# Kernel optimization log

Measured on AMD Instinct MI355X. Metric: run time of the kernel, lower is better.

Reference implementation:

```python
import jax, jax.numpy as jnp
import numpy as np

H = 1024
N_HEAD = 16
HEAD = H // N_HEAD
EPS = 1e-12


def setup_inputs() -> dict:
    key = jax.random.key(0)
    ks = jax.random.split(key, 12)
    B, S = 2, 2048
    scale = 1.0 / np.sqrt(H)
    inp = {
        "pre_out": jax.random.normal(ks[0], (B, S, H), dtype=jnp.float32),
        "att_mask": jnp.ones((B, 1, 1, S), dtype=jnp.float32),
        "Wq": jax.random.normal(ks[1], (H, H), dtype=jnp.float32) * scale,
        "bq": jnp.zeros((H,), dtype=jnp.float32),
        "Wk": jax.random.normal(ks[2], (H, H), dtype=jnp.float32) * scale,
        "bk": jnp.zeros((H,), dtype=jnp.float32),
        "Wv": jax.random.normal(ks[3], (H, H), dtype=jnp.float32) * scale,
        "bv": jnp.zeros((H,), dtype=jnp.float32),
        "Wo": jax.random.normal(ks[4], (H, H), dtype=jnp.float32) * scale,
        "bo": jnp.zeros((H,), dtype=jnp.float32),
        "ln_w": jnp.ones((H,), dtype=jnp.float32),
        "ln_b": jnp.zeros((H,), dtype=jnp.float32),
    }
    return inp


def _heads(x):
    # [B,S,H] -> [B,n_head,S,head]
    B, S, _ = x.shape
    return x.reshape(B, S, N_HEAD, HEAD).transpose(0, 2, 1, 3)


def _layernorm(x, w, b):
    u = jnp.mean(x, axis=-1, keepdims=True)
    s = jnp.mean((x - u) ** 2, axis=-1, keepdims=True)
    return w * ((x - u) / jnp.sqrt(s + EPS)) + b


def reference(pre_out, att_mask, Wq, bq, Wk, bk, Wv, bv, Wo, bo, ln_w, ln_b):
    B, S, _ = pre_out.shape
    # torch Linear: y = x @ W.T + b
    Q = _heads(pre_out @ Wq.T + bq)
    K = _heads(pre_out @ Wk.T + bk)
    V = _heads(pre_out @ Wv.T + bv)
    scores = jnp.einsum('bhqd,bhkd->bhqk', Q, K) / np.sqrt(HEAD)
    scores = scores + (1.0 - att_mask) * -10000.0
    prob = jax.nn.softmax(scores, axis=-1)  # eval mode: no dropout
    att = jnp.einsum('bhqk,bhkd->bhqd', prob, V)
    att = att.transpose(0, 2, 1, 3).reshape(B, S, H)
    out = att @ Wo.T + bo
    return _layernorm(pre_out + out, ln_w, ln_b)
```

## Files before the change

kernel.cpp:

```cpp
#include <hip/hip_runtime.h>
#include <math.h>

typedef unsigned short u16;
typedef float floatx4 __attribute__((ext_vector_type(4)));
typedef __bf16 bf16x8 __attribute__((ext_vector_type(8)));
typedef u16 u16x4 __attribute__((ext_vector_type(4)));

#define BB 2
#define SS 2048
#define HH 1024
#define NHEAD 16

__device__ __forceinline__ u16 f2bf(float f) {
  union { float f; unsigned u; } a; a.f = f;
  unsigned r = a.u + 0x7fffu + ((a.u >> 16) & 1u);
  return (u16)(r >> 16);
}

__device__ __forceinline__ u16 bfbits(float f) {
  union { __bf16 h; u16 u; } c; c.h = (__bf16)f; return c.u;
}

__device__ __forceinline__ float bf2f(u16 u) {
  union { unsigned u; float f; } a; a.u = ((unsigned)u) << 16; return a.f;
}

__device__ __forceinline__ void gload16(const u16* g, u16* l) {
  __builtin_amdgcn_global_load_lds((const __attribute__((address_space(1))) void*)g,
                                   (__attribute__((address_space(3))) void*)l, 16, 0, 0);
}

__global__ __launch_bounds__(256) void cvt_all(
    const float* __restrict__ X, const float* __restrict__ Wq, const float* __restrict__ Wk,
    const float* __restrict__ Wv, const float* __restrict__ Wo, const float* __restrict__ mask,
    u16* __restrict__ Xb, u16* __restrict__ Wqb, u16* __restrict__ Wkb,
    u16* __restrict__ Wvb, u16* __restrict__ Wob, float* __restrict__ B2) {
  int i = blockIdx.x * 256 + threadIdx.x;
  if (i >= (2 << 20)) {
    int off = i - (2 << 20);
    float4 m = ((const float4*)mask)[off];
    float4 o;
    o.x = (1.0f - m.x) * (-10000.0f * 1.44269504f);
    o.y = (1.0f - m.y) * (-10000.0f * 1.44269504f);
    o.z = (1.0f - m.z) * (-10000.0f * 1.44269504f);
    o.w = (1.0f - m.w) * (-10000.0f * 1.44269504f);
    ((float4*)B2)[off] = o;
    return;
  }
  const float* src; u16* dst; int off;
  if (i < (1 << 20)) { src = X; dst = Xb; off = i; }
  else {
    int j = i - (1 << 20);
    int m = j >> 18; off = j & ((1 << 18) - 1);
    src = (m == 0) ? Wq : (m == 1) ? Wk : (m == 2) ? Wv : Wo;
    dst = (m == 0) ? Wqb : (m == 1) ? Wkb : (m == 2) ? Wvb : Wob;
  }
  float4 v = ((const float4*)src)[off];
  u16x4 p; p.x = f2bf(v.x); p.y = f2bf(v.y); p.z = f2bf(v.z); p.w = f2bf(v.w);
  ((u16x4*)dst)[off] = p;
}

__global__ __launch_bounds__(256) void qkv_gemm(
    const u16* __restrict__ X,
    const u16* __restrict__ Wq, const u16* __restrict__ Wk, const u16* __restrict__ Wv,
    const float* __restrict__ bq, const float* __restrict__ bk, const float* __restrict__ bv,
    u16* __restrict__ Qo, u16* __restrict__ Ko, u16* __restrict__ Vt) {
  __shared__ u16 As[128 * 32];
  __shared__ u16 Ws[128 * 32];

  const int tid = threadIdx.x;
  const int w = tid >> 6, lane = tid & 63, quad = lane >> 4, l15 = lane & 15;
  const int mat = blockIdx.x >> 3;
  const int col0 = (blockIdx.x & 7) * 128;
  const int row0 = blockIdx.y * 128;
  const u16* W = (mat == 0) ? Wq : (mat == 1) ? Wk : Wv;
  const float* bias = (mat == 0) ? bq : (mat == 1) ? bk : bv;

  const int c0 = tid, c1 = tid + 256;
  const int ar0 = c0 >> 2, al0 = ((c0 & 3) ^ (ar0 & 3)) * 8;
  const int ar1 = c1 >> 2, al1 = ((c1 & 3) ^ (ar1 & 3)) * 8;
  const u16* gA0 = X + (row0 + ar0) * HH + al0;
  const u16* gA1 = X + (row0 + ar1) * HH + al1;
  const u16* gW0 = W + (col0 + ar0) * HH + al0;
  const u16* gW1 = W + (col0 + ar1) * HH + al1;
  u16* lA0 = As + c0 * 8; u16* lA1 = As + c1 * 8;
  u16* lW0 = Ws + c0 * 8; u16* lW1 = Ws + c1 * 8;

  const int wm = (w >> 1) * 64, wn = (w & 1) * 64;
  const int sw = quad ^ (l15 & 3);
  const int aoff = (wm + l15) * 32 + sw * 8;
  const int boff = (wn + l15) * 32 + sw * 8;

  floatx4 acc[4][4];
#pragma unroll
  for (int i = 0; i < 4; i++)
#pragma unroll
    for (int j = 0; j < 4; j++) acc[i][j] = {0.f, 0.f, 0.f, 0.f};

  for (int k0 = 0; k0 < HH; k0 += 32) {
    __syncthreads();
    gload16(gA0 + k0, lA0);
    gload16(gA1 + k0, lA1);
    gload16(gW0 + k0, lW0);
    gload16(gW1 + k0, lW1);
    __syncthreads();
    bf16x8 af[4], bfr[4];
#pragma unroll
    for (int i = 0; i < 4; i++) af[i] = *(const bf16x8*)(As + aoff + i * 512);
#pragma unroll
    for (int j = 0; j < 4; j++) bfr[j] = *(const bf16x8*)(Ws + boff + j * 512);
#pragma unroll
    for (int i = 0; i < 4; i++)
#pragma unroll
      for (int j = 0; j < 4; j++)
        acc[i][j] = __builtin_amdgcn_mfma_f32_16x16x32_bf16(af[i], bfr[j], acc[i][j], 0, 0, 0);
  }

  const int rb = row0 + wm + quad * 4;
  if (mat < 2) {
    u16* O = (mat == 0) ? Qo : Ko;
#pragma unroll
    for (int j = 0; j < 4; j++) {
      const int col = col0 + wn + j * 16 + l15;
      const float bj = bias[col];
#pragma unroll
      for (int i = 0; i < 4; i++) {
        const int r0 = rb + i * 16;
#pragma unroll
        for (int r = 0; r < 4; r++)
          O[(r0 + r) * HH + col] = bfbits(acc[i][j][r] + bj);
      }
    }
  } else {
#pragma unroll
    for (int j = 0; j < 4; j++) {
      const int col = col0 + wn + j * 16 + l15;
      const float bj = bias[col];
      const int h = col >> 6, d = col & 63;
#pragma unroll
      for (int i = 0; i < 4; i++) {
        const int m0 = rb + i * 16;
        const int b = m0 >> 11, s = m0 & 2047;
        u16x4 pk;
#pragma unroll
        for (int r = 0; r < 4; r++) pk[r] = bfbits(acc[i][j][r] + bj);
        *(u16x4*)(Vt + (((b * NHEAD + h) * 64 + d) * SS + s)) = pk;
      }
    }
  }
}

__global__ __launch_bounds__(256) void oproj_gemm(
    const u16* __restrict__ A, const u16* __restrict__ W,
    const float* __restrict__ bias, float* __restrict__ Y) {
  __shared__ u16 As[128 * 32];
  __shared__ u16 Ws[128 * 32];

  const int tid = threadIdx.x;
  const int w = tid >> 6, lane = tid & 63, quad = lane >> 4, l15 = lane & 15;
  const int col0 = blockIdx.x * 128;
  const int row0 = blockIdx.y * 128;

  const int c0 = tid, c1 = tid + 256;
  const int ar0 = c0 >> 2, al0 = ((c0 & 3) ^ (ar0 & 3)) * 8;
  const int ar1 = c1 >> 2, al1 = ((c1 & 3) ^ (ar1 & 3)) * 8;
  const u16* gA0 = A + (row0 + ar0) * HH + al0;
  const u16* gA1 = A + (row0 + ar1) * HH + al1;
  const u16* gW0 = W + (col0 + ar0) * HH + al0;
  const u16* gW1 = W + (col0 + ar1) * HH + al1;
  u16* lA0 = As + c0 * 8; u16* lA1 = As + c1 * 8;
  u16* lW0 = Ws + c0 * 8; u16* lW1 = Ws + c1 * 8;

  const int wm = (w >> 1) * 64, wn = (w & 1) * 64;
  const int sw = quad ^ (l15 & 3);
  const int aoff = (wm + l15) * 32 + sw * 8;
  const int boff = (wn + l15) * 32 + sw * 8;

  floatx4 acc[4][4];
#pragma unroll
  for (int i = 0; i < 4; i++)
#pragma unroll
    for (int j = 0; j < 4; j++) acc[i][j] = {0.f, 0.f, 0.f, 0.f};

  for (int k0 = 0; k0 < HH; k0 += 32) {
    __syncthreads();
    gload16(gA0 + k0, lA0);
    gload16(gA1 + k0, lA1);
    gload16(gW0 + k0, lW0);
    gload16(gW1 + k0, lW1);
    __syncthreads();
    bf16x8 af[4], bfr[4];
#pragma unroll
    for (int i = 0; i < 4; i++) af[i] = *(const bf16x8*)(As + aoff + i * 512);
#pragma unroll
    for (int j = 0; j < 4; j++) bfr[j] = *(const bf16x8*)(Ws + boff + j * 512);
#pragma unroll
    for (int i = 0; i < 4; i++)
#pragma unroll
      for (int j = 0; j < 4; j++)
        acc[i][j] = __builtin_amdgcn_mfma_f32_16x16x32_bf16(af[i], bfr[j], acc[i][j], 0, 0, 0);
  }

  const int rb = row0 + wm + quad * 4;
#pragma unroll
  for (int j = 0; j < 4; j++) {
    const int col = col0 + wn + j * 16 + l15;
    const float bj = bias[col];
#pragma unroll
    for (int i = 0; i < 4; i++) {
      const int r0 = rb + i * 16;
#pragma unroll
      for (int r = 0; r < 4; r++)
        Y[(r0 + r) * HH + col] = acc[i][j][r] + bj;
    }
  }
}

#define QT 128

__global__ __launch_bounds__(256) void attn_mfma(
    const u16* __restrict__ Q, const u16* __restrict__ K, const u16* __restrict__ Vt,
    const float* __restrict__ B2,
    u16* __restrict__ Po0, u16* __restrict__ Po1,
    float* __restrict__ L0, float* __restrict__ L1) {
  __shared__ u16 UQ[9216];
  __shared__ u16 Ks[64 * 64];
  __shared__ u16 Vs[64 * 64];

  const int qt = blockIdx.x, bh = blockIdx.y, split = blockIdx.z;
  const int b = bh >> 4, h = bh & 15;
  const int tid = threadIdx.x;
  const int w = tid >> 6, lane = tid & 63, quad = lane >> 4, l15 = lane & 15;
  const int sw = l15 & 7;

  u16* Po = split ? Po1 : Po0;
  float* Lp = split ? L1 : L0;

  const int qbase  = (b * SS + qt * QT) * HH + h * 64;
  const int kvbase = (b * SS) * HH + h * 64;
  const int vtbase = (b * NHEAD + h) * 64 * SS;

#pragma unroll
  for (int i = 0; i < 4; i++) {
    const int c = tid + i * 256;
    const int r = c >> 3, lc = (c & 7) ^ (r & 7);
    gload16(Q + qbase + r * HH + lc * 8, UQ + c * 8);
  }
  __syncthreads();

  bf16x8 aQ[2][2];
#pragma unroll
  for (int mt = 0; mt < 2; mt++) {
    const u16* qr = UQ + (w * 32 + mt * 16 + l15) * 64;
    aQ[mt][0] = *(const bf16x8*)(qr + ((quad ^ sw) * 8));
    aQ[mt][1] = *(const bf16x8*)(qr + (((4 + quad) ^ sw) * 8));
  }

  floatx4 o[2][4];
  float lp[2][4];
#pragma unroll
  for (int mt = 0; mt < 2; mt++)
#pragma unroll
    for (int j = 0; j < 4; j++) o[mt][j] = {0.f, 0.f, 0.f, 0.f};
#pragma unroll
  for (int mt = 0; mt < 2; mt++)
#pragma unroll
    for (int r = 0; r < 4; r++) lp[mt][r] = 0.f;

  u16* Pw = UQ + w * 2304;
  const float* B2row = B2 + b * SS;

  const int kt0 = split * 16;
  for (int kt = kt0; kt < kt0 + 16; kt++) {
    __syncthreads();
#pragma unroll
    for (int i = 0; i < 2; i++) {
      const int c = tid + i * 256;
      const int r = c >> 3, lc = (c & 7) ^ (r & 7);
      gload16(K + kvbase + (kt * 64 + r) * HH + lc * 8, Ks + c * 8);
      gload16(Vt + vtbase + r * SS + kt * 64 + lc * 8, Vs + c * 8);
    }
    __syncthreads();

    floatx4 s[2][4];
#pragma unroll
    for (int j = 0; j < 4; j++) {
      const u16* kr = Ks + (j * 16 + l15) * 64;
      bf16x8 b0 = *(const bf16x8*)(kr + ((quad ^ sw) * 8));
      bf16x8 b1 = *(const bf16x8*)(kr + (((4 + quad) ^ sw) * 8));
#pragma unroll
      for (int mt = 0; mt < 2; mt++) {
        floatx4 z = {0.f, 0.f, 0.f, 0.f};
        z = __builtin_amdgcn_mfma_f32_16x16x32_bf16(aQ[mt][0], b0, z, 0, 0, 0);
        s[mt][j] = __builtin_amdgcn_mfma_f32_16x16x32_bf16(aQ[mt][1], b1, z, 0, 0, 0);
      }
    }

#pragma unroll
    for (int j = 0; j < 4; j++) {
      const float bb = B2row[kt * 64 + j * 16 + l15];
#pragma unroll
      for (int mt = 0; mt < 2; mt++)
#pragma unroll
        for (int r = 0; r < 4; r++) {
          const float p = __builtin_amdgcn_exp2f(s[mt][j][r] * 0.180336880f + bb);
          s[mt][j][r] = p;
          lp[mt][r] += p;
        }
    }

#pragma unroll
    for (int mt = 0; mt < 2; mt++)
#pragma unroll
      for (int j = 0; j < 4; j++)
#pragma unroll
        for (int r = 0; r < 4; r++)
          Pw[(mt * 16 + quad * 4 + r) * 72 + j * 16 + l15] = bfbits(s[mt][j][r]);

    bf16x8 pa[2][2];
#pragma unroll
    for (int mt = 0; mt < 2; mt++) {
      const u16* pr = Pw + (mt * 16 + l15) * 72;
      pa[mt][0] = *(const bf16x8*)(pr + quad * 8);
      pa[mt][1] = *(const bf16x8*)(pr + 32 + quad * 8);
    }
#pragma unroll
    for (int j = 0; j < 4; j++) {
      const u16* vr = Vs + (j * 16 + l15) * 64;
      bf16x8 v0 = *(const bf16x8*)(vr + ((quad ^ sw) * 8));
      bf16x8 v1 = *(const bf16x8*)(vr + (((4 + quad) ^ sw) * 8));
#pragma unroll
      for (int mt = 0; mt < 2; mt++) {
        o[mt][j] = __builtin_amdgcn_mfma_f32_16x16x32_bf16(pa[mt][0], v0, o[mt][j], 0, 0, 0);
        o[mt][j] = __builtin_amdgcn_mfma_f32_16x16x32_bf16(pa[mt][1], v1, o[mt][j], 0, 0, 0);
      }
    }
  }

#pragma unroll
  for (int mt = 0; mt < 2; mt++)
#pragma unroll
    for (int r = 0; r < 4; r++) {
      float v = lp[mt][r];
      v += __shfl_xor(v, 1); v += __shfl_xor(v, 2);
      v += __shfl_xor(v, 4); v += __shfl_xor(v, 8);
      lp[mt][r] = v;
    }

#pragma unroll
  for (int mt = 0; mt < 2; mt++) {
    const int orow0 = b * SS + qt * QT + w * 32 + mt * 16 + quad * 4;
#pragma unroll
    for (int r = 0; r < 4; r++)
#pragma unroll
      for (int j = 0; j < 4; j++)
        Po[(orow0 + r) * HH + h * 64 + j * 16 + l15] = bfbits(o[mt][j][r]);
  }
  if (l15 == 0) {
#pragma unroll
    for (int mt = 0; mt < 2; mt++) {
      const int orow0 = b * SS + qt * QT + w * 32 + mt * 16 + quad * 4;
#pragma unroll
      for (int r = 0; r < 4; r++)
        Lp[(orow0 + r) * NHEAD + h] = lp[mt][r];
    }
  }
}

__global__ __launch_bounds__(256) void attn_combine(
    const u16* __restrict__ Po1, const float* __restrict__ L0,
    const float* __restrict__ L1, u16* __restrict__ Ab ) {
  const int idx = blockIdx.x * 256 + threadIdx.x;
  const int i = idx * 4;
  const int row = i >> 10;
  const int h = (i & 1023) >> 6;
  const float inv = 1.0f / (L0[row * NHEAD + h] + L1[row * NHEAD + h]);
  u16x4 a = ((const u16x4*)Ab)[idx];
  u16x4 c = ((const u16x4*)Po1)[idx];
  u16x4 o;
#pragma unroll
  for (int k = 0; k < 4; k++) o[k] = bfbits((bf2f(a[k]) + bf2f(c[k])) * inv);
  ((u16x4*)Ab)[idx] = o;
}

__device__ __forceinline__ float block_sum256(float v) {
  __shared__ float sb[4];
#pragma unroll
  for (int o = 1; o < 64; o <<= 1) v += __shfl_xor(v, o);
  if ((threadIdx.x & 63) == 0) sb[threadIdx.x >> 6] = v;
  __syncthreads();
  float r = sb[0] + sb[1] + sb[2] + sb[3];
  __syncthreads();
  return r;
}

__global__ __launch_bounds__(256) void add_layernorm(
    const float* __restrict__ x0, const float* __restrict__ y,
    const float* __restrict__ w, const float* __restrict__ b,
    float* __restrict__ out) {
  const int row = blockIdx.x;
  const int t = threadIdx.x;
  const float* xr = x0 + (size_t)row * HH;
  const float* yr = y + (size_t)row * HH;

  float v[4];
  float sum = 0.f;
#pragma unroll
  for (int i = 0; i < 4; i++) {
    int idx = t + i * 256;
    v[i] = xr[idx] + yr[idx];
    sum += v[i];
  }
  float mean = block_sum256(sum) * (1.0f / HH);

  float sq = 0.f;
#pragma unroll
  for (int i = 0; i < 4; i++) {
    float d = v[i] - mean;
    sq += d * d;
  }
  float var = block_sum256(sq) * (1.0f / HH);
  float inv = rsqrtf(var + 1e-12f);

#pragma unroll
  for (int i = 0; i < 4; i++) {
    int idx = t + i * 256;
    out[(size_t)row * HH + idx] = w[idx] * ((v[i] - mean) * inv) + b[idx];
  }
}

extern "C" void kernel_launch(void* const* d_in, const int* in_sizes, int n_in,
                              void* d_out, int out_size, void* d_ws, size_t ws_size,
                              hipStream_t stream) {
  const float* pre_out = (const float*)d_in[0];
  const float* mask    = (const float*)d_in[1];
  const float* Wq = (const float*)d_in[2];
  const float* bq = (const float*)d_in[3];
  const float* Wk = (const float*)d_in[4];
  const float* bk = (const float*)d_in[5];
  const float* Wv = (const float*)d_in[6];
  const float* bv = (const float*)d_in[7];
  const float* Wo = (const float*)d_in[8];
  const float* bo = (const float*)d_in[9];
  const float* ln_w = (const float*)d_in[10];
  const float* ln_b = (const float*)d_in[11];
  float* out = (float*)d_out;

  u16* Xb  = (u16*)d_ws;
  u16* Wqb = Xb + (4 << 20);
  u16* Wkb = Wqb + (1 << 20);
  u16* Wvb = Wkb + (1 << 20);
  u16* Wob = Wvb + (1 << 20);
  u16* Qb  = Wob + (1 << 20);
  u16* Kb  = Qb + (4 << 20);
  u16* Vtb = Kb + (4 << 20);
  u16* Ab  = Vtb + (4 << 20);
  float* Yb = (float*)(Ab + (4 << 20));
  float* B2 = Yb + (4 << 20);

  u16* Po1  = (u16*)Yb;
  float* L0 = (float*)(Po1 + (4 << 20));
  float* L1 = L0 + (BB * SS * NHEAD);

  cvt_all<<<8196, 256, 0, stream>>>(pre_out, Wq, Wk, Wv, Wo, mask,
                                    Xb, Wqb, Wkb, Wvb, Wob, B2);

  qkv_gemm<<<dim3(24, 32), 256, 0, stream>>>(Xb, Wqb, Wkb, Wvb, bq, bk, bv, Qb, Kb, Vtb);

  attn_mfma<<<dim3(SS / QT, BB * NHEAD, 2), 256, 0, stream>>>(Qb, Kb, Vtb, B2,
                                                              Ab, Po1, L0, L1);

  attn_combine<<<4096, 256, 0, stream>>>(Po1, L0, L1, Ab);

  oproj_gemm<<<dim3(8, 32), 256, 0, stream>>>(Ab, Wob, bo, Yb);

  add_layernorm<<<BB * SS, 256, 0, stream>>>(pre_out, Yb, ln_w, ln_b, out);
}
```

Measured before the change: 239.4 us.

## Double-buffer K/V tiles and keep P in registers via transposed score MFMA

The attention kernel now double-buffers K and V tiles in shared memory, prefetching the next tile while computing the current one, which removes one barrier per iteration. It also computes S^T (K as the A operand) so each lane holds probabilities in a layout that feeds 16x16x16 bf16 MFMAs directly, dropping the LDS round trip for P. Output stores become packed 4-wide writes and the row-sum reduction shrinks to two shuffles. The costs are twice the K/V LDS footprint and twice as many smaller MFMAs for the PV product.

Result: slower. 251.0 us (+4.8%).

```diff
diff --git a/kernel.cpp b/kernel.cpp
--- a/kernel.cpp
+++ b/kernel.cpp
@@ -4,6 +4,8 @@
 typedef unsigned short u16;
 typedef float floatx4 __attribute__((ext_vector_type(4)));
 typedef __bf16 bf16x8 __attribute__((ext_vector_type(8)));
+typedef __bf16 bf16x4 __attribute__((ext_vector_type(4)));
+typedef short s16x4 __attribute__((ext_vector_type(4)));
 typedef u16 u16x4 __attribute__((ext_vector_type(4)));
 
 #define BB 2
@@ -23,6 +25,15 @@
 
 __device__ __forceinline__ float bf2f(u16 u) {
   union { unsigned u; float f; } a; a.u = ((unsigned)u) << 16; return a.f;
+}
+
+__device__ __forceinline__ floatx4 mfma16(s16x4 a, s16x4 b, floatx4 c) {
+#if __has_builtin(__builtin_amdgcn_mfma_f32_16x16x16_bf16)
+  return __builtin_amdgcn_mfma_f32_16x16x16_bf16(
+      __builtin_bit_cast(bf16x4, a), __builtin_bit_cast(bf16x4, b), c, 0, 0, 0);
+#else
+  return __builtin_amdgcn_mfma_f32_16x16x16bf16_1k(a, b, c, 0, 0, 0);
+#endif
 }
 
 __device__ __forceinline__ void gload16(const u16* g, u16* l) {
@@ -223,9 +234,9 @@
     const float* __restrict__ B2,
     u16* __restrict__ Po0, u16* __restrict__ Po1,
     float* __restrict__ L0, float* __restrict__ L1) {
-  __shared__ u16 UQ[9216];
-  __shared__ u16 Ks[64 * 64];
-  __shared__ u16 Vs[64 * 64];
+  __shared__ u16 UQ[QT * 64];
+  __shared__ u16 Ks[2][64 * 64];
+  __shared__ u16 Vs[2][64 * 64];
 
   const int qt = blockIdx.x, bh = blockIdx.y, split = blockIdx.z;
   const int b = bh >> 4, h = bh & 15;
@@ -239,6 +250,7 @@
   const int qbase  = (b * SS + qt * QT) * HH + h * 64;
   const int kvbase = (b * SS) * HH + h * 64;
   const int vtbase = (b * NHEAD + h) * 64 * SS;
+  const int kt0 = split * 16;
 
 #pragma unroll
   for (int i = 0; i < 4; i++) {
@@ -246,6 +258,13 @@
     const int r = c >> 3, lc = (c & 7) ^ (r & 7);
     gload16(Q + qbase + r * HH + lc * 8, UQ + c * 8);
   }
+#pragma unroll
+  for (int i = 0; i < 2; i++) {
+    const int c = tid + i * 256;
+    const int r = c >> 3, lc = (c & 7) ^ (r & 7);
+    gload16(K + kvbase + (kt0 * 64 + r) * HH + lc * 8, Ks[0] + c * 8);
+    gload16(Vt + vtbase + r * SS + kt0 * 64 + lc * 8, Vs[0] + c * 8);
+  }
   __syncthreads();
 
   bf16x8 aQ[2][2];
@@ -257,113 +276,90 @@
   }
 
   floatx4 o[2][4];
-  float lp[2][4];
 #pragma unroll
   for (int mt = 0; mt < 2; mt++)
 #pragma unroll
-    for (int j = 0; j < 4; j++) o[mt][j] = {0.f, 0.f, 0.f, 0.f};
-#pragma unroll
-  for (int mt = 0; mt < 2; mt++)
-#pragma unroll
-    for (int r = 0; r < 4; r++) lp[mt][r] = 0.f;
-
-  u16* Pw = UQ + w * 2304;
+    for (int dt = 0; dt < 4; dt++) o[mt][dt] = {0.f, 0.f, 0.f, 0.f};
+  float lp[2] = {0.f, 0.f};
   const float* B2row = B2 + b * SS;
 
-  const int kt0 = split * 16;
-  for (int kt = kt0; kt < kt0 + 16; kt++) {
+  for (int it = 0; it < 16; it++) {
+    const int cur = it & 1;
     __syncthreads();
-#pragma unroll
-    for (int i = 0; i < 2; i++) {
-      const int c = tid + i * 256;
-      const int r = c >> 3, lc = (c & 7) ^ (r & 7);
-      gload16(K + kvbase + (kt * 64 + r) * HH + lc * 8, Ks + c * 8);
-      gload16(Vt + vtbase + r * SS + kt * 64 + lc * 8, Vs + c * 8);
-    }
-    __syncthreads();
-
-    floatx4 s[2][4];
-#pragma unroll
-    for (int j = 0; j < 4; j++) {
-      const u16* kr = Ks + (j * 16 + l15) * 64;
-      bf16x8 b0 = *(const bf16x8*)(kr + ((quad ^ sw) * 8));
-      bf16x8 b1 = *(const bf16x8*)(kr + (((4 + quad) ^ sw) * 8));
+    if (it < 15) {
+      const int kt = kt0 + it + 1;
+#pragma unroll
+      for (int i = 0; i < 2; i++) {
+        const int c = tid + i * 256;
+        const int r = c >> 3, lc = (c & 7) ^ (r & 7);
+        gload16(K + kvbase + (kt * 64 + r) * HH + lc * 8, Ks[cur ^ 1] + c * 8);
+        gload16(Vt + vtbase + r * SS + kt * 64 + lc * 8, Vs[cur ^ 1] + c * 8);
+      }
+    }
+    const int kt = kt0 + it;
+
+    floatx4 st[2][4];
+#pragma unroll
+    for (int kb = 0; kb < 4; kb++) {
+      const u16* kr = Ks[cur] + (kb * 16 + l15) * 64;
+      bf16x8 kf0 = *(const bf16x8*)(kr + ((quad ^ sw) * 8));
+      bf16x8 kf1 = *(const bf16x8*)(kr + (((4 + quad) ^ sw) * 8));
 #pragma unroll
       for (int mt = 0; mt < 2; mt++) {
         floatx4 z = {0.f, 0.f, 0.f, 0.f};
-        z = __builtin_amdgcn_mfma_f32_16x16x32_bf16(aQ[mt][0], b0, z, 0, 0, 0);
-        s[mt][j] = __builtin_amdgcn_mfma_f32_16x16x32_bf16(aQ[mt][1], b1, z, 0, 0, 0);
+        z = __builtin_amdgcn_mfma_f32_16x16x32_bf16(kf0, aQ[mt][0], z, 0, 0, 0);
+        st[mt][kb] = __builtin_amdgcn_mfma_f32_16x16x32_bf16(kf1, aQ[mt][1], z, 0, 0, 0);
       }
     }
 
-#pragma unroll
-    for (int j = 0; j < 4; j++) {
-      const float bb = B2row[kt * 64 + j * 16 + l15];
+    s16x4 pb[2][4];
+#pragma unroll
+    for (int kb = 0; kb < 4; kb++) {
+      const floatx4 bb = *(const floatx4*)(B2row + kt * 64 + kb * 16 + quad * 4);
 #pragma unroll
       for (int mt = 0; mt < 2; mt++)
 #pragma unroll
         for (int r = 0; r < 4; r++) {
-          const float p = __builtin_amdgcn_exp2f(s[mt][j][r] * 0.180336880f + bb);
-          s[mt][j][r] = p;
-          lp[mt][r] += p;
+          const float p = __builtin_amdgcn_exp2f(st[mt][kb][r] * 0.180336880f + bb[r]);
+          lp[mt] += p;
+          pb[mt][kb][r] = (short)bfbits(p);
         }
     }
 
 #pragma unroll
-    for (int mt = 0; mt < 2; mt++)
-#pragma unroll
-      for (int j = 0; j < 4; j++)
-#pragma unroll
-        for (int r = 0; r < 4; r++)
-          Pw[(mt * 16 + quad * 4 + r) * 72 + j * 16 + l15] = bfbits(s[mt][j][r]);
-
-    bf16x8 pa[2][2];
-#pragma unroll
-    for (int mt = 0; mt < 2; mt++) {
-      const u16* pr = Pw + (mt * 16 + l15) * 72;
-      pa[mt][0] = *(const bf16x8*)(pr + quad * 8);
-      pa[mt][1] = *(const bf16x8*)(pr + 32 + quad * 8);
-    }
-#pragma unroll
-    for (int j = 0; j < 4; j++) {
-      const u16* vr = Vs + (j * 16 + l15) * 64;
-      bf16x8 v0 = *(const bf16x8*)(vr + ((quad ^ sw) * 8));
-      bf16x8 v1 = *(const bf16x8*)(vr + (((4 + quad) ^ sw) * 8));
-#pragma unroll
-      for (int mt = 0; mt < 2; mt++) {
-        o[mt][j] = __builtin_amdgcn_mfma_f32_16x16x32_bf16(pa[mt][0], v0, o[mt][j], 0, 0, 0);
-        o[mt][j] = __builtin_amdgcn_mfma_f32_16x16x32_bf16(pa[mt][1], v1, o[mt][j], 0, 0, 0);
+    for (int dt = 0; dt < 4; dt++) {
+      const u16* vr = Vs[cur] + (dt * 16 + l15) * 64;
+#pragma unroll
+      for (int kb = 0; kb < 4; kb++) {
+        const int pc = (2 * kb + (quad >> 1)) ^ sw;
+        s16x4 va = *(const s16x4*)(vr + pc * 8 + (quad & 1) * 4);
+#pragma unroll
+        for (int mt = 0; mt < 2; mt++)
+          o[mt][dt] = mfma16(va, pb[mt][kb], o[mt][dt]);
       }
     }
   }
 
 #pragma unroll
-  for (int mt = 0; mt < 2; mt++)
-#pragma unroll
-    for (int r = 0; r < 4; r++) {
-      float v = lp[mt][r];
-      v += __shfl_xor(v, 1); v += __shfl_xor(v, 2);
-      v += __shfl_xor(v, 4); v += __shfl_xor(v, 8);
-      lp[mt][r] = v;
-    }
-
-#pragma unroll
   for (int mt = 0; mt < 2; mt++) {
-    const int orow0 = b * SS + qt * QT + w * 32 + mt * 16 + quad * 4;
-#pragma unroll
-    for (int r = 0; r < 4; r++)
-#pragma unroll
-      for (int j = 0; j < 4; j++)
-        Po[(orow0 + r) * HH + h * 64 + j * 16 + l15] = bfbits(o[mt][j][r]);
-  }
-  if (l15 == 0) {
-#pragma unroll
-    for (int mt = 0; mt < 2; mt++) {
-      const int orow0 = b * SS + qt * QT + w * 32 + mt * 16 + quad * 4;
-#pragma unroll
-      for (int r = 0; r < 4; r++)
-        Lp[(orow0 + r) * NHEAD + h] = lp[mt][r];
-    }
+    float v = lp[mt];
+    v += __shfl_xor(v, 16);
+    v += __shfl_xor(v, 32);
+    lp[mt] = v;
+  }
+
+#pragma unroll
+  for (int mt = 0; mt < 2; mt++) {
+    const int qrow = b * SS + qt * QT + w * 32 + mt * 16 + l15;
+    u16* orow = Po + qrow * HH + h * 64;
+#pragma unroll
+    for (int dt = 0; dt < 4; dt++) {
+      u16x4 pk;
+#pragma unroll
+      for (int r = 0; r < 4; r++) pk[r] = bfbits(o[mt][dt][r]);
+      *(u16x4*)(orow + dt * 16 + quad * 4) = pk;
+    }
+    if (lane < 16) Lp[qrow * NHEAD + h] = lp[mt];
   }
 }
 
```
